# Kernel tuning notes

Hardware: AMD Instinct MI355X
Metric: run time of the kernel (lower is better)

The kernel has to match this reference:

```python
import jax, jax.numpy as jnp
import numpy as np

EPS = 1e-5

def layernorm(x, gamma, beta):
    mu = jnp.mean(x, axis=-1, keepdims=True)
    var = jnp.mean(jnp.square(x - mu), axis=-1, keepdims=True)
    return (x - mu) * jax.lax.rsqrt(var + EPS) * gamma + beta

def setup_inputs() -> dict:
    key = jax.random.key(0)
    ks = jax.random.split(key, 5)
    B, I, H = 8192, 1024, 1024
    x = jax.random.normal(ks[0], (B, I), dtype=jnp.float32)
    hx = jax.random.normal(ks[1], (B, H), dtype=jnp.float32)
    cx = jax.random.normal(ks[2], (B, H), dtype=jnp.float32)
    W_ih = jax.random.normal(ks[3], (4 * H, I), dtype=jnp.float32)
    W_hh = jax.random.normal(ks[4], (4 * H, H), dtype=jnp.float32)
    gamma_i = jnp.ones((4 * H,), jnp.float32); beta_i = jnp.zeros((4 * H,), jnp.float32)
    gamma_h = jnp.ones((4 * H,), jnp.float32); beta_h = jnp.zeros((4 * H,), jnp.float32)
    gamma_c = jnp.ones((H,), jnp.float32); beta_c = jnp.zeros((H,), jnp.float32)
    return {"x": x, "hx": hx, "cx": cx, "W_ih": W_ih, "W_hh": W_hh,
            "gamma_i": gamma_i, "beta_i": beta_i,
            "gamma_h": gamma_h, "beta_h": beta_h,
            "gamma_c": gamma_c, "beta_c": beta_c}

def reference(x, hx, cx, W_ih, W_hh, gamma_i, beta_i, gamma_h, beta_h, gamma_c, beta_c):
    # igates/hgates: [B, 4H]
    igates = layernorm(x @ W_ih.T, gamma_i, beta_i)
    hgates = layernorm(hx @ W_hh.T, gamma_h, beta_h)
    gates = igates + hgates
    i, f, g, o = jnp.split(gates, 4, axis=1)
    i = jax.nn.sigmoid(i)
    f = jax.nn.sigmoid(f)
    g = jnp.tanh(g)
    o = jax.nn.sigmoid(o)
    cy = layernorm(f * cx + i * g, gamma_c, beta_c)
    hy = o * jnp.tanh(cy)
    return (hy, (hy, cy))
```

## Files before the change

### kernel.cpp

```cpp
#include <hip/hip_runtime.h>

typedef __attribute__((ext_vector_type(8))) short short8_t;
typedef __attribute__((ext_vector_type(4))) float f32x4;

#define AS1 __attribute__((address_space(1)))
#define AS3 __attribute__((address_space(3)))

__device__ inline void gload_lds16(const void* g, void* l) {
  __builtin_amdgcn_global_load_lds((AS1 void*)g, (AS3 void*)l, 16, 0, 0);
}

__device__ inline unsigned short f2bf(float f) {
  unsigned int u = __builtin_bit_cast(unsigned int, f);
  u += 0x7fffu + ((u >> 16) & 1u);
  return (unsigned short)(u >> 16);
}
__device__ inline float bfu2f(unsigned short u) {
  return __builtin_bit_cast(float, ((unsigned int)u) << 16);
}
__device__ inline float sigmoidf_(float x) {
  x = fminf(fmaxf(x, -30.f), 30.f);
  return 1.f / (1.f + __expf(-x));
}
__device__ inline float tanhf_(float x) {
  x = fminf(fmaxf(x, -15.f), 15.f);
  float e = __expf(2.f * x);
  return (e - 1.f) / (e + 1.f);
}

__global__ __launch_bounds__(256) void cvt_bf16(const float* __restrict__ src,
                                                unsigned short* __restrict__ dst,
                                                int n) {
  int i = (blockIdx.x * 256 + threadIdx.x) * 8;
  if (i >= n) return;
  const float4* s = reinterpret_cast<const float4*>(src + i);
  float4 a = s[0], b = s[1];
  union { unsigned short us[8]; uint4 v; } o;
  o.us[0] = f2bf(a.x); o.us[1] = f2bf(a.y); o.us[2] = f2bf(a.z); o.us[3] = f2bf(a.w);
  o.us[4] = f2bf(b.x); o.us[5] = f2bf(b.y); o.us[6] = f2bf(b.z); o.us[7] = f2bf(b.w);
  *reinterpret_cast<uint4*>(dst + i) = o.v;
}

__global__ __launch_bounds__(256) void gemm_dual(
    const unsigned short* __restrict__ Xb, const unsigned short* __restrict__ Hxb,
    const unsigned short* __restrict__ Wib, const unsigned short* __restrict__ Whb,
    unsigned short* __restrict__ Gi, unsigned short* __restrict__ Gh) {
  const int K = 1024, N = 4096;
  const unsigned short* A  = blockIdx.z ? Hxb : Xb;
  const unsigned short* Bw = blockIdx.z ? Whb : Wib;
  unsigned short* C        = blockIdx.z ? Gh : Gi;

  __shared__ __align__(16) unsigned short lA[128 * 32];
  __shared__ __align__(16) unsigned short lB[128 * 32];

  const int t    = threadIdx.x;
  const int wid  = t >> 6;
  const int lane = t & 63;
  const int m0 = blockIdx.y * 128, n0 = blockIdx.x * 128;
  const int wm = (wid >> 1) * 64, wn = (wid & 1) * 64;
  const int fr = lane & 15, fq = lane >> 4;

  f32x4 acc[4][4];
#pragma unroll
  for (int i = 0; i < 4; ++i)
#pragma unroll
    for (int j = 0; j < 4; ++j) acc[i][j] = (f32x4){0.f, 0.f, 0.f, 0.f};

  for (int k0 = 0; k0 < K; k0 += 32) {
#pragma unroll
    for (int c = 0; c < 2; ++c) {
      int idx = c * 256 + t;
      int row = idx >> 2;
      int kp  = (idx & 3) << 3;
      const unsigned short* ga = A  + (size_t)(m0 + row) * K + (k0 + kp);
      const unsigned short* gb = Bw + (size_t)(n0 + row) * K + (k0 + kp);
      unsigned short* la = (unsigned short*)lA + c * 2048 + wid * 512;
      unsigned short* lb = (unsigned short*)lB + c * 2048 + wid * 512;
      gload_lds16(ga, la);
      gload_lds16(gb, lb);
    }
    __syncthreads();

    short8_t av[4], bv[4];
#pragma unroll
    for (int i = 0; i < 4; ++i) {
      av[i] = *reinterpret_cast<const short8_t*>(&lA[(wm + i * 16 + fr) * 32 + fq * 8]);
      bv[i] = *reinterpret_cast<const short8_t*>(&lB[(wn + i * 16 + fr) * 32 + fq * 8]);
    }
#pragma unroll
    for (int i = 0; i < 4; ++i)
#pragma unroll
      for (int j = 0; j < 4; ++j)
        acc[i][j] = __builtin_amdgcn_mfma_f32_16x16x32_bf16(av[i], bv[j], acc[i][j], 0, 0, 0);
    __syncthreads();
  }

#pragma unroll
  for (int i = 0; i < 4; ++i)
#pragma unroll
    for (int j = 0; j < 4; ++j)
#pragma unroll
      for (int r = 0; r < 4; ++r) {
        int row = m0 + wm + i * 16 + fq * 4 + r;
        int col = n0 + wn + j * 16 + fr;
        C[(size_t)row * N + col] = f2bf(acc[i][j][r]);
      }
}

__global__ __launch_bounds__(256) void fuse_ln_lstm(
    const unsigned short* __restrict__ Gi, const unsigned short* __restrict__ Gh,
    const float* __restrict__ cx,
    const float* __restrict__ gi_g, const float* __restrict__ gi_b,
    const float* __restrict__ gh_g, const float* __restrict__ gh_b,
    const float* __restrict__ gc_g, const float* __restrict__ gc_b,
    float* __restrict__ out) {
  const int H = 1024;
  const size_t BH = (size_t)8192 * 1024;
  const int b = blockIdx.x, t = threadIdx.x;
  const int wid = t >> 6, lane = t & 63;

  __shared__ __align__(16) unsigned short lgi[4096];
  __shared__ __align__(16) unsigned short lgh[4096];
  __shared__ float lred[32];

  const uint4* gi_row = reinterpret_cast<const uint4*>(Gi) + (size_t)b * 512;
  const uint4* gh_row = reinterpret_cast<const uint4*>(Gh) + (size_t)b * 512;

  float si = 0.f, qi = 0.f, sh = 0.f, qh = 0.f;
#pragma unroll
  for (int c = 0; c < 2; ++c) {
    uint4 v = gi_row[c * 256 + t];
    uint4 w = gh_row[c * 256 + t];
    *reinterpret_cast<uint4*>(&lgi[(c * 256 + t) * 8]) = v;
    *reinterpret_cast<uint4*>(&lgh[(c * 256 + t) * 8]) = w;
    unsigned int uv[4] = {v.x, v.y, v.z, v.w};
    unsigned int uw[4] = {w.x, w.y, w.z, w.w};
#pragma unroll
    for (int e = 0; e < 4; ++e) {
      float a0 = __builtin_bit_cast(float, uv[e] << 16);
      float a1 = __builtin_bit_cast(float, uv[e] & 0xffff0000u);
      si += a0 + a1; qi += a0 * a0 + a1 * a1;
      float b0 = __builtin_bit_cast(float, uw[e] << 16);
      float b1 = __builtin_bit_cast(float, uw[e] & 0xffff0000u);
      sh += b0 + b1; qh += b0 * b0 + b1 * b1;
    }
  }
#pragma unroll
  for (int s = 32; s; s >>= 1) {
    si += __shfl_xor(si, s); qi += __shfl_xor(qi, s);
    sh += __shfl_xor(sh, s); qh += __shfl_xor(qh, s);
  }
  if (lane == 0) { lred[wid] = si; lred[4 + wid] = qi; lred[8 + wid] = sh; lred[12 + wid] = qh; }
  __syncthreads();
  float Si = lred[0] + lred[1] + lred[2] + lred[3];
  float Qi = lred[4] + lred[5] + lred[6] + lred[7];
  float Sh = lred[8] + lred[9] + lred[10] + lred[11];
  float Qh = lred[12] + lred[13] + lred[14] + lred[15];
  const float inv4096 = 1.f / 4096.f;
  float mui = Si * inv4096;
  float rsi = rsqrtf(fmaxf(Qi * inv4096 - mui * mui, 0.f) + 1e-5f);
  float muh = Sh * inv4096;
  float rsh = rsqrtf(fmaxf(Qh * inv4096 - muh * muh, 0.f) + 1e-5f);

  float cv[4], ov[4];
  float sc = 0.f, qc = 0.f;
#pragma unroll
  for (int k = 0; k < 4; ++k) {
    int h = t + 256 * k;
    float g0 = bfu2f(lgi[h]),        h0 = bfu2f(lgh[h]);
    float g1 = bfu2f(lgi[h + 1024]), h1 = bfu2f(lgh[h + 1024]);
    float g2 = bfu2f(lgi[h + 2048]), h2 = bfu2f(lgh[h + 2048]);
    float g3 = bfu2f(lgi[h + 3072]), h3 = bfu2f(lgh[h + 3072]);
    float vi = (g0 - mui) * rsi * gi_g[h]        + gi_b[h]        + (h0 - muh) * rsh * gh_g[h]        + gh_b[h];
    float vf = (g1 - mui) * rsi * gi_g[h + 1024] + gi_b[h + 1024] + (h1 - muh) * rsh * gh_g[h + 1024] + gh_b[h + 1024];
    float vg = (g2 - mui) * rsi * gi_g[h + 2048] + gi_b[h + 2048] + (h2 - muh) * rsh * gh_g[h + 2048] + gh_b[h + 2048];
    float vo = (g3 - mui) * rsi * gi_g[h + 3072] + gi_b[h + 3072] + (h3 - muh) * rsh * gh_g[h + 3072] + gh_b[h + 3072];
    float ig = sigmoidf_(vi), fg = sigmoidf_(vf), gg = tanhf_(vg), og = sigmoidf_(vo);
    float c = fg * cx[(size_t)b * H + h] + ig * gg;
    cv[k] = c; ov[k] = og;
    sc += c; qc += c * c;
  }
#pragma unroll
  for (int s = 32; s; s >>= 1) { sc += __shfl_xor(sc, s); qc += __shfl_xor(qc, s); }
  if (lane == 0) { lred[16 + wid] = sc; lred[20 + wid] = qc; }
  __syncthreads();
  float Sc = lred[16] + lred[17] + lred[18] + lred[19];
  float Qc = lred[20] + lred[21] + lred[22] + lred[23];
  const float inv1024 = 1.f / 1024.f;
  float muc = Sc * inv1024;
  float rsc = rsqrtf(fmaxf(Qc * inv1024 - muc * muc, 0.f) + 1e-5f);
#pragma unroll
  for (int k = 0; k < 4; ++k) {
    int h = t + 256 * k;
    float cy = (cv[k] - muc) * rsc * gc_g[h] + gc_b[h];
    float hy = ov[k] * tanhf_(cy);
    size_t o0 = (size_t)b * H + h;
    out[o0] = hy;
    out[BH + o0] = hy;
    out[2 * BH + o0] = cy;
  }
}

extern "C" void kernel_launch(void* const* d_in, const int* in_sizes, int n_in,
                              void* d_out, int out_size, void* d_ws, size_t ws_size,
                              hipStream_t stream) {
  const float* x    = (const float*)d_in[0];
  const float* hx   = (const float*)d_in[1];
  const float* cx   = (const float*)d_in[2];
  const float* Wih  = (const float*)d_in[3];
  const float* Whh  = (const float*)d_in[4];
  const float* gi_g = (const float*)d_in[5];
  const float* gi_b = (const float*)d_in[6];
  const float* gh_g = (const float*)d_in[7];
  const float* gh_b = (const float*)d_in[8];
  const float* gc_g = (const float*)d_in[9];
  const float* gc_b = (const float*)d_in[10];
  float* out = (float*)d_out;

  const size_t NB = (size_t)8192 * 1024;
  const size_t NW = (size_t)4096 * 1024;
  const size_t NG = (size_t)8192 * 4096;

  unsigned short* ws  = (unsigned short*)d_ws;
  unsigned short* xb  = ws;
  unsigned short* hxb = xb + NB;
  unsigned short* wib = hxb + NB;
  unsigned short* whb = wib + NW;
  unsigned short* Gi  = whb + NW;
  unsigned short* Gh  = Gi + NG;

  cvt_bf16<<<(int)(NB / 2048), 256, 0, stream>>>(x, xb, (int)NB);
  cvt_bf16<<<(int)(NB / 2048), 256, 0, stream>>>(hx, hxb, (int)NB);
  cvt_bf16<<<(int)(NW / 2048), 256, 0, stream>>>(Wih, wib, (int)NW);
  cvt_bf16<<<(int)(NW / 2048), 256, 0, stream>>>(Whh, whb, (int)NW);

  dim3 gg(4096 / 128, 8192 / 128, 2);
  gemm_dual<<<gg, 256, 0, stream>>>(xb, hxb, wib, whb, Gi, Gh);

  fuse_ln_lstm<<<8192, 256, 0, stream>>>(Gi, Gh, cx, gi_g, gi_b, gh_g, gh_b,
                                         gc_g, gc_b, out);
}
```

Measured before the change: 267.9 us.

## Enlarge GEMM tile to 256x256 with triple-buffered LDS prefetch and swizzle

The dual bf16 GEMM moves from 128x128 tiles with 256 threads to 256x256 tiles with 512 threads, so each wave computes a 64x128 sub-tile. LDS becomes a 3-stage ring filled by async global_load_lds two k-steps ahead, with vmcnt waits and one barrier per step in place of the two syncthreads. An XOR swizzle on the k-chunk is added to cut LDS bank conflicts, and MFMA issue is raised in priority. The cost is more accumulator registers and 96KB of LDS per block, which limits occupancy, and a grid of 1024 blocks.

```diff
diff --git a/kernel.cpp b/kernel.cpp
--- a/kernel.cpp
+++ b/kernel.cpp
@@ -41,7 +41,7 @@
   *reinterpret_cast<uint4*>(dst + i) = o.v;
 }
 
-__global__ __launch_bounds__(256) void gemm_dual(
+__global__ __launch_bounds__(512, 2) void gemm_dual(
     const unsigned short* __restrict__ Xb, const unsigned short* __restrict__ Hxb,
     const unsigned short* __restrict__ Wib, const unsigned short* __restrict__ Whb,
     unsigned short* __restrict__ Gi, unsigned short* __restrict__ Gh) {
@@ -50,59 +50,95 @@
   const unsigned short* Bw = blockIdx.z ? Whb : Wib;
   unsigned short* C        = blockIdx.z ? Gh : Gi;
 
-  __shared__ __align__(16) unsigned short lA[128 * 32];
-  __shared__ __align__(16) unsigned short lB[128 * 32];
+  __shared__ __align__(16) unsigned short lA[3 * 256 * 32];
+  __shared__ __align__(16) unsigned short lB[3 * 256 * 32];
 
   const int t    = threadIdx.x;
   const int wid  = t >> 6;
   const int lane = t & 63;
-  const int m0 = blockIdx.y * 128, n0 = blockIdx.x * 128;
-  const int wm = (wid >> 1) * 64, wn = (wid & 1) * 64;
   const int fr = lane & 15, fq = lane >> 4;
-
-  f32x4 acc[4][4];
-#pragma unroll
-  for (int i = 0; i < 4; ++i)
-#pragma unroll
-    for (int j = 0; j < 4; ++j) acc[i][j] = (f32x4){0.f, 0.f, 0.f, 0.f};
-
-  for (int k0 = 0; k0 < K; k0 += 32) {
-#pragma unroll
-    for (int c = 0; c < 2; ++c) {
-      int idx = c * 256 + t;
+  const int m0 = blockIdx.y * 256, n0 = blockIdx.x * 256;
+  const int wrb = (wid >> 1) * 64;
+  const int wcb = (wid & 1) * 128;
+
+  auto stage = [&](int kt, int sbuf) {
+    const int k0 = kt * 32;
+#pragma unroll
+    for (int g = 0; g < 2; ++g) {
+      int idx = g * 512 + t;
       int row = idx >> 2;
-      int kp  = (idx & 3) << 3;
-      const unsigned short* ga = A  + (size_t)(m0 + row) * K + (k0 + kp);
-      const unsigned short* gb = Bw + (size_t)(n0 + row) * K + (k0 + kp);
-      unsigned short* la = (unsigned short*)lA + c * 2048 + wid * 512;
-      unsigned short* lb = (unsigned short*)lB + c * 2048 + wid * 512;
+      int ls  = (idx & 3) ^ ((idx >> 3) & 3);
+      const unsigned short* ga = A  + (size_t)(m0 + row) * K + k0 + ls * 8;
+      const unsigned short* gb = Bw + (size_t)(n0 + row) * K + k0 + ls * 8;
+      unsigned short* la = lA + sbuf * 8192 + g * 4096 + wid * 512;
+      unsigned short* lb = lB + sbuf * 8192 + g * 4096 + wid * 512;
       gload_lds16(ga, la);
       gload_lds16(gb, lb);
     }
-    __syncthreads();
-
-    short8_t av[4], bv[4];
-#pragma unroll
-    for (int i = 0; i < 4; ++i) {
-      av[i] = *reinterpret_cast<const short8_t*>(&lA[(wm + i * 16 + fr) * 32 + fq * 8]);
-      bv[i] = *reinterpret_cast<const short8_t*>(&lB[(wn + i * 16 + fr) * 32 + fq * 8]);
-    }
+  };
+
+  f32x4 acc[4][8];
+#pragma unroll
+  for (int i = 0; i < 4; ++i)
+#pragma unroll
+    for (int j = 0; j < 8; ++j) acc[i][j] = (f32x4){0.f, 0.f, 0.f, 0.f};
+
+  stage(0, 0);
+  stage(1, 1);
+  asm volatile("s_waitcnt vmcnt(4)" ::: "memory");
+  __builtin_amdgcn_sched_barrier(0);
+  __builtin_amdgcn_s_barrier();
+  __builtin_amdgcn_sched_barrier(0);
+
+  const int NT = K / 32;
+  const int swz = (fq ^ ((fr >> 1) & 3)) * 8;
+
+  int cur = 0;
+  for (int kt = 0; kt < NT; ++kt) {
+    if (kt + 2 < NT) {
+      int n2 = cur + 2; if (n2 >= 3) n2 -= 3;
+      stage(kt + 2, n2);
+    }
+    const unsigned short* a_base = lA + cur * 8192;
+    const unsigned short* b_base = lB + cur * 8192;
+
+    short8_t bv[8], av[4];
+#pragma unroll
+    for (int j = 0; j < 8; ++j)
+      bv[j] = *reinterpret_cast<const short8_t*>(b_base + (wcb + j * 16 + fr) * 32 + swz);
 #pragma unroll
     for (int i = 0; i < 4; ++i)
-#pragma unroll
-      for (int j = 0; j < 4; ++j)
+      av[i] = *reinterpret_cast<const short8_t*>(a_base + (wrb + i * 16 + fr) * 32 + swz);
+
+    __builtin_amdgcn_s_setprio(1);
+#pragma unroll
+    for (int i = 0; i < 4; ++i)
+#pragma unroll
+      for (int j = 0; j < 8; ++j)
         acc[i][j] = __builtin_amdgcn_mfma_f32_16x16x32_bf16(av[i], bv[j], acc[i][j], 0, 0, 0);
-    __syncthreads();
+    __builtin_amdgcn_s_setprio(0);
+
+    if (kt < NT - 1) {
+      if (kt + 2 < NT) {
+        asm volatile("s_waitcnt vmcnt(4)" ::: "memory");
+      } else {
+        asm volatile("s_waitcnt vmcnt(0)" ::: "memory");
+      }
+      __builtin_amdgcn_sched_barrier(0);
+      __builtin_amdgcn_s_barrier();
+      __builtin_amdgcn_sched_barrier(0);
+    }
+    cur = (cur + 1 == 3) ? 0 : cur + 1;
   }
 
 #pragma unroll
   for (int i = 0; i < 4; ++i)
 #pragma unroll
-    for (int j = 0; j < 4; ++j)
+    for (int j = 0; j < 8; ++j)
 #pragma unroll
       for (int r = 0; r < 4; ++r) {
-        int row = m0 + wm + i * 16 + fq * 4 + r;
-        int col = n0 + wn + j * 16 + fr;
+        int row = m0 + wrb + i * 16 + fq * 4 + r;
+        int col = n0 + wcb + j * 16 + fr;
         C[(size_t)row * N + col] = f2bf(acc[i][j][r]);
       }
 }
@@ -234,8 +270,8 @@
   cvt_bf16<<<(int)(NW / 2048), 256, 0, stream>>>(Wih, wib, (int)NW);
   cvt_bf16<<<(int)(NW / 2048), 256, 0, stream>>>(Whh, whb, (int)NW);
 
-  dim3 gg(4096 / 128, 8192 / 128, 2);
-  gemm_dual<<<gg, 256, 0, stream>>>(xb, hxb, wib, whb, Gi, Gh);
+  dim3 gg(4096 / 256, 8192 / 256, 2);
+  gemm_dual<<<gg, 512, 0, stream>>>(xb, hxb, wib, whb, Gi, Gh);
 
   fuse_ln_lstm<<<8192, 256, 0, stream>>>(Gi, Gh, cx, gi_g, gi_b, gh_g, gh_b,
                                          gc_g, gc_b, out);
```

Result: slower. 275.6 us (+2.9%).
